# Performance work log

Hardware: AMD Instinct MI355X
Metric: run time of the kernel (lower is better)

## Reference

```python
import jax, jax.numpy as jnp
import numpy as np

SAMPLE_RATE = 22050
N_FILTER_BANKS = 64
HOP_LENGTH = 512
BATCH = 4
N_FRAMES = 500
N_SAMPLES = N_FRAMES * HOP_LENGTH


def _frame_mean_weights(n_frames, n_samples):
    """Per-frame weights w s.t. mean over time of linear(align_corners=True)
    upsampling of a length-n_frames signal equals w @ signal (exact same math,
    since the interpolation is linear in the frame values)."""
    pos = jnp.linspace(0.0, n_frames - 1.0, n_samples)
    lo = jnp.clip(jnp.floor(pos).astype(jnp.int32), 0, n_frames - 2)
    frac = pos - lo
    w = jnp.zeros(n_frames, dtype=jnp.float32)
    w = w.at[lo].add(1.0 - frac).at[lo + 1].add(frac)
    return w / n_samples


def setup_inputs() -> dict:
    key = jax.random.key(0)
    k1, k2 = jax.random.split(key)
    filter_magnitudes = jax.random.uniform(k1, (BATCH, N_FRAMES, N_FILTER_BANKS), dtype=jnp.float32)
    noise = jax.random.normal(k2, (BATCH, N_SAMPLES), dtype=jnp.float32)
    return {"filter_magnitudes": filter_magnitudes, "noise": noise}


def reference(filter_magnitudes, noise):
    B, n_frames, n_banks = filter_magnitudes.shape
    n_samples = noise.shape[1]

    noise_fft = jnp.fft.rfft(noise, axis=1)                      # (B, n_freq) complex
    freqs = jnp.fft.rfftfreq(n_samples, 1.0 / SAMPLE_RATE)       # (n_freq,)
    filter_freqs = jnp.logspace(np.log10(20.0), np.log10(SAMPLE_RATE / 2.0), n_banks).astype(jnp.float32)

    # mean over time of the linearly-upsampled magnitudes (exact, no big buffer)
    mean_w = _frame_mean_weights(n_frames, n_samples)            # (n_frames,)
    mean_mag = jnp.einsum('bfk,f->bk', filter_magnitudes, mean_w)  # (B, n_banks)

    # vectorized log-distance filterbank weights: (n_freq, n_banks)
    D = jnp.log(freqs + 1e-7)[:, None] - jnp.log(filter_freqs + 1e-7)[None, :]
    W = jnp.exp(-(D ** 2) / 0.5)
    W = W / (W.sum(axis=1, keepdims=True) + 1e-7)

    filter_response = mean_mag @ W.T                              # (B, n_freq)
    filtered_fft = noise_fft * filter_response
    return jnp.fft.irfft(filtered_fft, n=n_samples, axis=1)      # (B, n_samples)
```

## Files before the change

### kernel.cpp

```cpp
#include <hip/hip_runtime.h>
#include <math.h>

#define NS 256000
#define N1 512
#define N2 500
#define PI_F 3.14159265358979323846f

typedef float2 cplx;

__device__ __forceinline__ cplx cadd(cplx a, cplx b){ return make_float2(a.x+b.x, a.y+b.y); }
__device__ __forceinline__ cplx csub(cplx a, cplx b){ return make_float2(a.x-b.x, a.y-b.y); }
__device__ __forceinline__ cplx cmul(cplx a, cplx b){ return make_float2(a.x*b.x-a.y*b.y, a.x*b.y+a.y*b.x); }
__device__ __forceinline__ cplx cmulc(cplx a, cplx b){ return make_float2(a.x*b.x+a.y*b.y, a.y*b.x-a.x*b.y); }
__device__ __forceinline__ cplx crotf(cplx v, float ang){
    float sn = __sinf(ang), cs = __cosf(ang);
    return make_float2(v.x*cs - v.y*sn, v.x*sn + v.y*cs);
}
__device__ __forceinline__ int PX(int e){ return e + (e>>4); }
__device__ __forceinline__ int rev8_3(int k){ return ((k&7)<<6) | (k&0x38) | (k>>6); }

#define U1PAD 545
#define U2PAD 537
#define WFENCE() asm volatile("s_waitcnt lgkmcnt(0)" ::: "memory")

template<bool INV>
__device__ __forceinline__ void dft4(const cplx* a, cplx* b){
    cplx t0=cadd(a[0],a[2]), t1=csub(a[0],a[2]), t2=cadd(a[1],a[3]), t3=csub(a[1],a[3]);
    b[0]=cadd(t0,t2); b[2]=csub(t0,t2);
    if(!INV){ b[1]=make_float2(t1.x+t3.y, t1.y-t3.x); b[3]=make_float2(t1.x-t3.y, t1.y+t3.x); }
    else    { b[1]=make_float2(t1.x-t3.y, t1.y+t3.x); b[3]=make_float2(t1.x+t3.y, t1.y-t3.x); }
}

template<bool INV>
__device__ __forceinline__ void dft8(const cplx* a, cplx* b){
    cplx ev[4]={a[0],a[2],a[4],a[6]}, od[4]={a[1],a[3],a[5],a[7]};
    cplx C[4], D[4];
    dft4<INV>(ev, C); dft4<INV>(od, D);
    const float s = 0.70710678118654752f;
    const float sg = INV ? 1.f : -1.f;
    cplx d1 = cmul(D[1], make_float2( s, sg*s));
    cplx d2 = cmul(D[2], make_float2(0.f, sg ));
    cplx d3 = cmul(D[3], make_float2(-s, sg*s));
    b[0]=cadd(C[0],D[0]); b[4]=csub(C[0],D[0]);
    b[1]=cadd(C[1],d1);   b[5]=csub(C[1],d1);
    b[2]=cadd(C[2],d2);   b[6]=csub(C[2],d2);
    b[3]=cadd(C[3],d3);   b[7]=csub(C[3],d3);
}

template<bool INV>
__device__ __forceinline__ void dft5(const cplx* a, cplx* b){
    const float c1=0.30901699437494742f, s1=0.95105651629515357f;
    const float c2=-0.80901699437494745f, s2=0.58778525229247312f;
    const float sg = INV ? 1.f : -1.f;
    cplx W[5];
    W[0]=make_float2(1.f,0.f);
    W[1]=make_float2(c1, sg*s1); W[2]=make_float2(c2, sg*s2);
    W[3]=make_float2(c2,-sg*s2); W[4]=make_float2(c1,-sg*s1);
#pragma unroll
    for(int u=0;u<5;++u){
        cplx acc = a[0];
        int idx = 0;
#pragma unroll
        for(int r=1;r<5;++r){
            idx += u; if(idx >= 5) idx -= 5;
            acc = cadd(acc, cmul(a[r], W[idx]));
        }
        b[u] = acc;
    }
}

template<int R, int L, int TMUL, bool INV, int NN>
__device__ __forceinline__ void wstage(cplx* Uw, const cplx* tab, int lane){
    constexpr int m = L / R;
    constexpr int nb = NN / R;
    constexpr int NIT = (nb + 63) / 64;
    cplx a[NIT][R];
    cplx wt[NIT][R];
    int  bs[NIT];
#pragma unroll
    for(int it=0; it<NIT; ++it){
        int beta = lane + it*64;
        int blk = beta / m;
        int j = beta - blk*m;
        bs[it] = blk*L + j;
        if(beta < nb){
#pragma unroll
            for(int t=0;t<R;++t) a[it][t] = Uw[PX(bs[it] + m*t)];
#pragma unroll
            for(int t=1;t<R;++t) wt[it][t] = tab[TMUL*j*t];
        }
    }
#pragma unroll
    for(int it=0; it<NIT; ++it){
        int beta = lane + it*64;
        if(beta < nb){
            if(INV){
#pragma unroll
                for(int t=1;t<R;++t) a[it][t] = cmulc(a[it][t], wt[it][t]);
            }
            cplx bb[R];
            if constexpr (R==4) dft4<INV>(a[it], bb);
            else if constexpr (R==5) dft5<INV>(a[it], bb);
            else dft8<INV>(a[it], bb);
            if(!INV){
#pragma unroll
                for(int t=1;t<R;++t) bb[t] = cmul(bb[t], wt[it][t]);
            }
#pragma unroll
            for(int t=0;t<R;++t) Uw[PX(bs[it] + m*t)] = bb[t];
        }
    }
}

template<int NTAB>
__device__ __forceinline__ void build_tab(cplx* tab, int tid){
    const float step = -2.f*PI_F/(float)NTAB;
    for(int i = tid; i < NTAB; i += 128){
        float a = step*(float)i;
        tab[i] = make_float2(__cosf(a), __sinf(a));
    }
}

__device__ __forceinline__ int p2k2(int p){
    int t1 = p/100; int r = p - 100*t1;
    int t2 = r/20;  r -= 20*t2;
    int t3 = r>>2;  int t4 = r & 3;
    return t1 + 5*t2 + 25*t3 + 125*t4;
}
__device__ __forceinline__ int k22p(int k){
    int t1 = k % 5; int k5 = k/5;
    int t2 = k5 % 5; int k25 = k5/5;
    int t3 = k25 % 5; int t4 = k25/5;
    return 100*t1 + 20*t2 + 4*t3 + t4;
}
__device__ __forceinline__ int colord(int q){
    int j = q>>1, w = q&1;
    if(j == 0) return w ? 256 : 0;
    return w ? 512 - j : j;
}
__device__ __forceinline__ int xcd_chunk(int bid, int n){
    int q = n>>3, r = n&7;
    int x = bid&7, idx = bid>>3;
    return (x < r ? x*(q+1) : r*(q+1) + (x-r)*q) + idx;
}

__device__ __forceinline__ void hpair(cplx Z1, cplx Z2, float ha, float hb,
                                      cplx* zk, cplx* znk){
    float xr = 0.5f*(Z1.x + Z2.x), xi = 0.5f*(Z1.y - Z2.y);
    float yr = 0.5f*(Z1.y + Z2.y), yi = -0.5f*(Z1.x - Z2.x);
    *zk  = make_float2(ha*xr - hb*yi, ha*xi + hb*yr);
    *znk = make_float2(ha*xr + hb*yi, hb*yr - ha*xi);
}

__global__ void __launch_bounds__(128) kFused1(const float* __restrict__ fm,
                                               const float* __restrict__ noise,
                                               float* __restrict__ mmL,
                                               cplx* __restrict__ Y){
    __shared__ float Aarr[500];
    __shared__ float wfr[500];
    __shared__ float part[128];
    __shared__ cplx tab[512];
    __shared__ cplx U[2][U1PAD];
    const int bid = blockIdx.x, tid = threadIdx.x;
    if(bid < 4){
        const int b = bid;
        for(int f = tid; f < 500; f += 128){
            long long i0 = ((long long)f*255999LL + 498LL)/499LL;
            long long i1 = ((long long)(f+1)*255999LL + 498LL)/499LL;
            long long cnt = i1 - i0;
            long long sumi = (i0 + i1 - 1)*cnt/2;
            long long num = 499LL*sumi - cnt*(long long)f*255999LL;
            Aarr[f] = (float)((double)num / 255999.0);
        }
        __syncthreads();
        for(int f = tid; f < 500; f += 128){
            long long i0 = ((long long)f*255999LL + 498LL)/499LL;
            long long i1 = ((long long)(f+1)*255999LL + 498LL)/499LL;
            double w;
            if(f < 499) w = (double)(i1 - i0) - (double)Aarr[f] + (f > 0 ? (double)Aarr[f-1] : 0.0);
            else        w = (double)Aarr[498] + 1.0;
            wfr[f] = (float)(w / (double)NS);
        }
        __syncthreads();
        const int k = tid & 63, seg = tid >> 6;
        float acc = 0.f;
        for(int f = seg*250; f < seg*250 + 250; ++f)
            acc += wfr[f] * fm[(b*500 + f)*64 + k];
        part[seg*64 + k] = acc;
        __syncthreads();
        if(tid < 64) mmL[b*64 + tid] = part[tid] + part[64 + tid];
        return;
    }
    if(bid == 4){
        if(tid < 64){
            double a = log10(20.0), b2 = log10(11025.0);
            double e = a + (b2 - a)*(double)tid/63.0;
            float ff = (float)pow(10.0, e);
            mmL[256 + tid] = logf(ff + 1e-7f);
        }
        return;
    }
    const int g = bid - 5;
    const int s = g / 250;
    const int n2base = (g - s*250) * 2;
    const int lane = tid & 63, w = tid >> 6;
    build_tab<512>(tab, tid);
    const float* xa = noise + (size_t)(2*s)*NS + n2base;
    const float* xb = noise + (size_t)(2*s+1)*NS + n2base;
#pragma unroll
    for(int k=0;k<8;++k){
        int i = tid + 128*k;
        int n1 = i >> 1, ws = i & 1;
        U[ws][PX(n1)] = make_float2(xa[n1*500 + ws], xb[n1*500 + ws]);
    }
    __syncthreads();
    cplx* Uw = U[w];
    wstage<8,512, 1,false,512>(Uw, tab, lane); WFENCE();
    wstage<8, 64, 8,false,512>(Uw, tab, lane); WFENCE();
    wstage<8,  8,64,false,512>(Uw, tab, lane); WFENCE();
    const int n2 = n2base + w;
    cplx* yp = Y + ((size_t)s*500 + n2)*512;
    const float tw = -2.f*PI_F/(float)NS;
#pragma unroll
    for(int t=0;t<8;++t){
        int q = lane + 64*t;
        int c = colord(q);
        cplx v = Uw[PX(rev8_3(c))];
        v = crotf(v, tw*(float)(n2*c));
        yp[q] = v;
    }
}

__global__ void __launch_bounds__(128) kFused2(cplx* __restrict__ Y,
                                               const float* __restrict__ mmL){
    __shared__ cplx tab[500];
    __shared__ cplx U[2][U2PAD];
    __shared__ float Hr[4][500];
    __shared__ float mmS[2][64];
    __shared__ float lgf[64];
    const int tid = threadIdx.x, lane = tid & 63, w = tid >> 6;
    const int L = xcd_chunk(blockIdx.x, 512);
    const int s = L >> 8, blk = L & 255;
    build_tab<500>(tab, tid);
    if(tid < 128) mmS[tid>>6][tid&63] = mmL[2*s*64 + tid];
    if(tid < 64)  lgf[tid] = mmL[256 + tid];
    cplx* yb = Y + (size_t)s*500*512 + 2*blk;
    cplx rg[8];
#pragma unroll
    for(int k=0;k<8;++k){
        int i = tid + 128*k;
        rg[k] = (i < 1000) ? yb[(i>>1)*512 + (i&1)] : make_float2(0.f, 0.f);
    }
    __syncthreads();
    const int nrows = (blk == 0) ? 2 : 1;
    const float invN = 1.f/(float)NS;
    for(int idx = tid; idx < nrows*500; idx += 128){
        int r = (idx >= 500) ? 1 : 0;
        int p = idx - 500*r;
        int k1 = (blk == 0) ? (r ? 256 : 0) : blk;
        int k2 = p2k2(p);
        int kf = k1 + 512*k2;
        int kk = min(kf, NS - kf);
        float lf = logf((float)kk*(22050.f/(float)NS) + 1e-7f);
        float wsum = 0.f, a0 = 0.f, a1 = 0.f;
#pragma unroll
        for(int jb=0;jb<64;++jb){
            float d = lf - lgf[jb];
            float e = __expf(-2.f*d*d);
            wsum += e; a0 += e*mmS[0][jb]; a1 += e*mmS[1][jb];
        }
        float inv = invN/(wsum + 1e-7f);
        Hr[2*r  ][p] = a0*inv;
        Hr[2*r+1][p] = a1*inv;
    }
#pragma unroll
    for(int k=0;k<8;++k){
        int i = tid + 128*k;
        if(i < 1000) U[i&1][PX(i>>1)] = rg[k];
    }
    __syncthreads();
    cplx* Uw = U[w];
    wstage<5,500,  1,false,500>(Uw, tab, lane); WFENCE();
    wstage<5,100,  5,false,500>(Uw, tab, lane); WFENCE();
    wstage<5, 20, 25,false,500>(Uw, tab, lane); WFENCE();
    wstage<4,  4,125,false,500>(Uw, tab, lane); WFENCE();
    __syncthreads();
    if(blk == 0){
        if(w == 0){
#pragma unroll
            for(int t=0;t<8;++t){
                int p = lane + 64*t;
                if(p < 500){
                    int k2 = p2k2(p);
                    int pp = k22p((500 - k2) % 500);
                    if(p <= pp){
                        cplx Z1 = U[0][PX(p)], Z2 = U[0][PX(pp)];
                        cplx zk, znk;
                        hpair(Z1, Z2, Hr[0][p], Hr[1][p], &zk, &znk);
                        U[0][PX(p)]  = zk;
                        U[0][PX(pp)] = znk;
                    }
                }
            }
        } else {
#pragma unroll
            for(int t=0;t<4;++t){
                int p = lane + 64*t;
                if(p < 250){
                    cplx Z1 = U[1][PX(p)], Z2 = U[1][PX(499-p)];
                    cplx zk, znk;
                    hpair(Z1, Z2, Hr[2][p], Hr[3][p], &zk, &znk);
                    U[1][PX(p)]     = zk;
                    U[1][PX(499-p)] = znk;
                }
            }
        }
    } else {
#pragma unroll
        for(int t=0;t<4;++t){
            int pl = lane + 64*t;
            if(pl < 250){
                int p = w*250 + pl;
                cplx Z1 = U[0][PX(p)], Z2 = U[1][PX(499-p)];
                cplx zk, znk;
                hpair(Z1, Z2, Hr[0][p], Hr[1][p], &zk, &znk);
                U[0][PX(p)]     = zk;
                U[1][PX(499-p)] = znk;
            }
        }
    }
    __syncthreads();
    wstage<4,  4,125,true,500>(Uw, tab, lane); WFENCE();
    wstage<5, 20, 25,true,500>(Uw, tab, lane); WFENCE();
    wstage<5,100,  5,true,500>(Uw, tab, lane); WFENCE();
    wstage<5,500,  1,true,500>(Uw, tab, lane); WFENCE();
    __syncthreads();
    const float tw = 2.f*PI_F/(float)NS;
#pragma unroll
    for(int k=0;k<8;++k){
        int i = tid + 128*k;
        if(i < 1000){
            int n2 = i >> 1, ws = i & 1;
            int c = colord(2*blk + ws);
            cplx v = U[ws][PX(n2)];
            v = crotf(v, tw*(float)(n2*c));
            yb[n2*512 + ws] = v;
        }
    }
}

__global__ void __launch_bounds__(128) kFused3(const cplx* __restrict__ Y,
                                               float* __restrict__ out){
    __shared__ cplx tab[512];
    __shared__ cplx U[2][U1PAD];
    const int tid = threadIdx.x, lane = tid & 63, w = tid >> 6;
    const int L = xcd_chunk(blockIdx.x, 500);
    const int s = L / 250;
    const int n2base = (L - s*250) * 2;
    build_tab<512>(tab, tid);
    const cplx* yp = Y + ((size_t)s*500 + n2base)*512;
#pragma unroll
    for(int k=0;k<8;++k){
        int i = tid + 128*k;
        int ws = i >> 9, q = i & 511;
        cplx v = yp[(size_t)ws*512 + q];
        U[ws][PX(rev8_3(colord(q)))] = v;
    }
    __syncthreads();
    cplx* Uw = U[w];
    wstage<8,  8,64,true,512>(Uw, tab, lane); WFENCE();
    wstage<8, 64, 8,true,512>(Uw, tab, lane); WFENCE();
    wstage<8,512, 1,true,512>(Uw, tab, lane); WFENCE();
    __syncthreads();
    float* oa = out + (size_t)(2*s)*NS + n2base;
    float* ob = out + (size_t)(2*s+1)*NS + n2base;
#pragma unroll
    for(int k=0;k<8;++k){
        int i = tid + 128*k;
        int n1 = i >> 1, ws = i & 1;
        cplx v = U[ws][PX(n1)];
        oa[n1*500 + ws] = v.x;
        ob[n1*500 + ws] = v.y;
    }
}

extern "C" void kernel_launch(void* const* d_in, const int* in_sizes, int n_in,
                              void* d_out, int out_size, void* d_ws, size_t ws_size,
                              hipStream_t stream) {
    const float* fm = (const float*)d_in[0];
    const float* noise = (const float*)d_in[1];
    float* out = (float*)d_out;

    char* ws = (char*)d_ws;
    cplx*  Y   = (cplx*)ws;
    float* mmL = (float*)(ws + 4200000);

    kFused1<<<505, 128, 0, stream>>>(fm, noise, mmL, Y);
    kFused2<<<512, 128, 0, stream>>>(Y, mmL);
    kFused3<<<500, 128, 0, stream>>>(Y, out);
}
```

Before: 98.65 us.

## Widen FFT blocks to four columns, pad Y rows, and roll FFT stage loops

kFused1 and kFused3 now use 256-thread blocks that each process four columns instead of two, and they remap block IDs across XCDs. The Y workspace row stride is padded from 512 to 528, presumably to reduce channel or bank conflicts. The templated radix stages are replaced by rolled per-wave FFT loops, and many unrolls are disabled to cut code size and register pressure. kFused2 now issues its global loads before building the twiddle table and uses a lighter barrier. The rolled loops may add loop overhead and lose instruction-level parallelism.

Measured after the change: 100.4 us. No clear change (+1.8%).

```diff
diff --git a/kernel.cpp b/kernel.cpp
--- a/kernel.cpp
+++ b/kernel.cpp
@@ -4,6 +4,7 @@
 #define NS 256000
 #define N1 512
 #define N2 500
+#define YS 528
 #define PI_F 3.14159265358979323846f
 
 typedef float2 cplx;
@@ -22,6 +23,7 @@
 #define U1PAD 545
 #define U2PAD 537
 #define WFENCE() asm volatile("s_waitcnt lgkmcnt(0)" ::: "memory")
+#define LDS_BARRIER() do{ asm volatile("s_waitcnt lgkmcnt(0)" ::: "memory"); __builtin_amdgcn_s_barrier(); }while(0)
 
 template<bool INV>
 __device__ __forceinline__ void dft4(const cplx* a, cplx* b){
@@ -69,53 +71,110 @@
     }
 }
 
-template<int R, int L, int TMUL, bool INV, int NN>
-__device__ __forceinline__ void wstage(cplx* Uw, const cplx* tab, int lane){
-    constexpr int m = L / R;
-    constexpr int nb = NN / R;
-    constexpr int NIT = (nb + 63) / 64;
-    cplx a[NIT][R];
-    cplx wt[NIT][R];
-    int  bs[NIT];
-#pragma unroll
-    for(int it=0; it<NIT; ++it){
-        int beta = lane + it*64;
-        int blk = beta / m;
-        int j = beta - blk*m;
-        bs[it] = blk*L + j;
-        if(beta < nb){
-#pragma unroll
-            for(int t=0;t<R;++t) a[it][t] = Uw[PX(bs[it] + m*t)];
-#pragma unroll
-            for(int t=1;t<R;++t) wt[it][t] = tab[TMUL*j*t];
-        }
-    }
-#pragma unroll
-    for(int it=0; it<NIT; ++it){
-        int beta = lane + it*64;
-        if(beta < nb){
-            if(INV){
-#pragma unroll
-                for(int t=1;t<R;++t) a[it][t] = cmulc(a[it][t], wt[it][t]);
-            }
-            cplx bb[R];
-            if constexpr (R==4) dft4<INV>(a[it], bb);
-            else if constexpr (R==5) dft5<INV>(a[it], bb);
-            else dft8<INV>(a[it], bb);
-            if(!INV){
-#pragma unroll
-                for(int t=1;t<R;++t) bb[t] = cmul(bb[t], wt[it][t]);
-            }
-#pragma unroll
-            for(int t=0;t<R;++t) Uw[PX(bs[it] + m*t)] = bb[t];
-        }
-    }
-}
-
-template<int NTAB>
+template<bool INV>
+__device__ __forceinline__ void fft512_wave(cplx* Uw, const cplx* tab, int lane){
+#pragma unroll 1
+    for(int st=0; st<3; ++st){
+        const int sh = INV ? 3*st : 6-3*st;
+        const int m = 1<<sh;
+        const int blk = lane >> sh, j = lane & (m-1);
+        const int base = (blk << (sh+3)) + j;
+        cplx a[8], wt[8];
+#pragma unroll
+        for(int t=0;t<8;++t) a[t] = Uw[PX(base + (t<<sh))];
+#pragma unroll
+        for(int t=1;t<8;++t) wt[t] = tab[(j*t) << (6-sh)];
+        if(INV){
+#pragma unroll
+            for(int t=1;t<8;++t) a[t] = cmulc(a[t], wt[t]);
+        }
+        cplx bb[8];
+        dft8<INV>(a,bb);
+        if(!INV){
+#pragma unroll
+            for(int t=1;t<8;++t) bb[t] = cmul(bb[t], wt[t]);
+        }
+#pragma unroll
+        for(int t=0;t<8;++t) Uw[PX(base + (t<<sh))] = bb[t];
+        WFENCE();
+    }
+}
+
+template<bool INV>
+__device__ __forceinline__ void fft500_wave(cplx* Uw, const cplx* tab, int lane){
+    if(INV){
+#pragma unroll 1
+        for(int it=0; it<2; ++it){
+            int beta = lane + 64*it;
+            if(beta < 125){
+                int base = beta*4;
+                cplx a[4];
+#pragma unroll
+                for(int t=0;t<4;++t) a[t] = Uw[PX(base+t)];
+                cplx bb[4];
+                dft4<true>(a,bb);
+#pragma unroll
+                for(int t=0;t<4;++t) Uw[PX(base+t)] = bb[t];
+            }
+        }
+        WFENCE();
+    }
+#pragma unroll 1
+    for(int s5=0; s5<3; ++s5){
+        const int st = INV ? 2-s5 : s5;
+        const int m  = (st==0)?100:((st==1)?20:4);
+        const int tm = (st==0)?1:((st==1)?5:25);
+#pragma unroll 1
+        for(int it=0; it<2; ++it){
+            int beta = lane + 64*it;
+            if(beta < 100){
+                int blk = (st==0) ? 0 : ((st==1) ? (int)(((unsigned)beta*52429u)>>20) : (beta>>2));
+                int j = beta - blk*m;
+                int base = blk*(m*5) + j;
+                cplx a[5], wt[5];
+#pragma unroll
+                for(int t=0;t<5;++t) a[t] = Uw[PX(base + m*t)];
+#pragma unroll
+                for(int t=1;t<5;++t) wt[t] = tab[tm*j*t];
+                if(INV){
+#pragma unroll
+                    for(int t=1;t<5;++t) a[t] = cmulc(a[t], wt[t]);
+                }
+                cplx bb[5];
+                dft5<INV>(a,bb);
+                if(!INV){
+#pragma unroll
+                    for(int t=1;t<5;++t) bb[t] = cmul(bb[t], wt[t]);
+                }
+#pragma unroll
+                for(int t=0;t<5;++t) Uw[PX(base + m*t)] = bb[t];
+            }
+        }
+        WFENCE();
+    }
+    if(!INV){
+#pragma unroll 1
+        for(int it=0; it<2; ++it){
+            int beta = lane + 64*it;
+            if(beta < 125){
+                int base = beta*4;
+                cplx a[4];
+#pragma unroll
+                for(int t=0;t<4;++t) a[t] = Uw[PX(base+t)];
+                cplx bb[4];
+                dft4<false>(a,bb);
+#pragma unroll
+                for(int t=0;t<4;++t) Uw[PX(base+t)] = bb[t];
+            }
+        }
+        WFENCE();
+    }
+}
+
+template<int NTAB, int NTHR>
 __device__ __forceinline__ void build_tab(cplx* tab, int tid){
     const float step = -2.f*PI_F/(float)NTAB;
-    for(int i = tid; i < NTAB; i += 128){
+    for(int i = tid; i < NTAB; i += NTHR){
         float a = step*(float)i;
         tab[i] = make_float2(__cosf(a), __sinf(a));
     }
@@ -152,19 +211,19 @@
     *znk = make_float2(ha*xr + hb*yi, hb*yr - ha*xi);
 }
 
-__global__ void __launch_bounds__(128) kFused1(const float* __restrict__ fm,
+__global__ void __launch_bounds__(256) kFused1(const float* __restrict__ fm,
                                                const float* __restrict__ noise,
                                                float* __restrict__ mmL,
                                                cplx* __restrict__ Y){
     __shared__ float Aarr[500];
     __shared__ float wfr[500];
-    __shared__ float part[128];
+    __shared__ float part[256];
     __shared__ cplx tab[512];
-    __shared__ cplx U[2][U1PAD];
+    __shared__ cplx U[4][U1PAD];
     const int bid = blockIdx.x, tid = threadIdx.x;
     if(bid < 4){
         const int b = bid;
-        for(int f = tid; f < 500; f += 128){
+        for(int f = tid; f < 500; f += 256){
             long long i0 = ((long long)f*255999LL + 498LL)/499LL;
             long long i1 = ((long long)(f+1)*255999LL + 498LL)/499LL;
             long long cnt = i1 - i0;
@@ -173,7 +232,7 @@
             Aarr[f] = (float)((double)num / 255999.0);
         }
         __syncthreads();
-        for(int f = tid; f < 500; f += 128){
+        for(int f = tid; f < 500; f += 256){
             long long i0 = ((long long)f*255999LL + 498LL)/499LL;
             long long i1 = ((long long)(f+1)*255999LL + 498LL)/499LL;
             double w;
@@ -184,11 +243,11 @@
         __syncthreads();
         const int k = tid & 63, seg = tid >> 6;
         float acc = 0.f;
-        for(int f = seg*250; f < seg*250 + 250; ++f)
+        for(int f = seg*125; f < seg*125 + 125; ++f)
             acc += wfr[f] * fm[(b*500 + f)*64 + k];
         part[seg*64 + k] = acc;
         __syncthreads();
-        if(tid < 64) mmL[b*64 + tid] = part[tid] + part[64 + tid];
+        if(tid < 64) mmL[b*64 + tid] = part[tid] + part[64+tid] + part[128+tid] + part[192+tid];
         return;
     }
     if(bid == 4){
@@ -200,28 +259,26 @@
         }
         return;
     }
-    const int g = bid - 5;
-    const int s = g / 250;
-    const int n2base = (g - s*250) * 2;
+    const int g = xcd_chunk(bid - 5, 250);
+    const int s = g / 125;
+    const int n2base = (g - s*125) * 4;
     const int lane = tid & 63, w = tid >> 6;
-    build_tab<512>(tab, tid);
+    build_tab<512,256>(tab, tid);
     const float* xa = noise + (size_t)(2*s)*NS + n2base;
     const float* xb = noise + (size_t)(2*s+1)*NS + n2base;
 #pragma unroll
     for(int k=0;k<8;++k){
-        int i = tid + 128*k;
-        int n1 = i >> 1, ws = i & 1;
+        int i = tid + 256*k;
+        int n1 = i >> 2, ws = i & 3;
         U[ws][PX(n1)] = make_float2(xa[n1*500 + ws], xb[n1*500 + ws]);
     }
     __syncthreads();
     cplx* Uw = U[w];
-    wstage<8,512, 1,false,512>(Uw, tab, lane); WFENCE();
-    wstage<8, 64, 8,false,512>(Uw, tab, lane); WFENCE();
-    wstage<8,  8,64,false,512>(Uw, tab, lane); WFENCE();
+    fft512_wave<false>(Uw, tab, lane);
     const int n2 = n2base + w;
-    cplx* yp = Y + ((size_t)s*500 + n2)*512;
+    cplx* yp = Y + ((size_t)s*500 + n2)*YS;
     const float tw = -2.f*PI_F/(float)NS;
-#pragma unroll
+#pragma unroll 1
     for(int t=0;t<8;++t){
         int q = lane + 64*t;
         int c = colord(q);
@@ -241,19 +298,20 @@
     const int tid = threadIdx.x, lane = tid & 63, w = tid >> 6;
     const int L = xcd_chunk(blockIdx.x, 512);
     const int s = L >> 8, blk = L & 255;
-    build_tab<500>(tab, tid);
+    cplx* yb = Y + (size_t)s*500*YS + 2*blk;
+    cplx rg[8];
+#pragma unroll
+    for(int k=0;k<8;++k){
+        int i = tid + 128*k;
+        rg[k] = (i < 1000) ? yb[(i>>1)*YS + (i&1)] : make_float2(0.f, 0.f);
+    }
+    build_tab<500,128>(tab, tid);
     if(tid < 128) mmS[tid>>6][tid&63] = mmL[2*s*64 + tid];
     if(tid < 64)  lgf[tid] = mmL[256 + tid];
-    cplx* yb = Y + (size_t)s*500*512 + 2*blk;
-    cplx rg[8];
-#pragma unroll
-    for(int k=0;k<8;++k){
-        int i = tid + 128*k;
-        rg[k] = (i < 1000) ? yb[(i>>1)*512 + (i&1)] : make_float2(0.f, 0.f);
-    }
-    __syncthreads();
+    LDS_BARRIER();
     const int nrows = (blk == 0) ? 2 : 1;
     const float invN = 1.f/(float)NS;
+#pragma unroll 1
     for(int idx = tid; idx < nrows*500; idx += 128){
         int r = (idx >= 500) ? 1 : 0;
         int p = idx - 500*r;
@@ -263,15 +321,15 @@
         int kk = min(kf, NS - kf);
         float lf = logf((float)kk*(22050.f/(float)NS) + 1e-7f);
         float wsum = 0.f, a0 = 0.f, a1 = 0.f;
-#pragma unroll
+#pragma unroll 8
         for(int jb=0;jb<64;++jb){
             float d = lf - lgf[jb];
             float e = __expf(-2.f*d*d);
             wsum += e; a0 += e*mmS[0][jb]; a1 += e*mmS[1][jb];
         }
         float inv = invN/(wsum + 1e-7f);
-        Hr[2*r  ][p] = a0*inv;
-        Hr[2*r+1][p] = a1*inv;
+        if(r==0){ Hr[0][p] = a0*inv; Hr[1][p] = a1*inv; }
+        else    { Hr[2][p] = a0*inv; Hr[3][p] = a1*inv; }
     }
 #pragma unroll
     for(int k=0;k<8;++k){
@@ -280,14 +338,11 @@
     }
     __syncthreads();
     cplx* Uw = U[w];
-    wstage<5,500,  1,false,500>(Uw, tab, lane); WFENCE();
-    wstage<5,100,  5,false,500>(Uw, tab, lane); WFENCE();
-    wstage<5, 20, 25,false,500>(Uw, tab, lane); WFENCE();
-    wstage<4,  4,125,false,500>(Uw, tab, lane); WFENCE();
+    fft500_wave<false>(Uw, tab, lane);
     __syncthreads();
     if(blk == 0){
         if(w == 0){
-#pragma unroll
+#pragma unroll 1
             for(int t=0;t<8;++t){
                 int p = lane + 64*t;
                 if(p < 500){
@@ -303,7 +358,7 @@
                 }
             }
         } else {
-#pragma unroll
+#pragma unroll 1
             for(int t=0;t<4;++t){
                 int p = lane + 64*t;
                 if(p < 250){
@@ -316,7 +371,7 @@
             }
         }
     } else {
-#pragma unroll
+#pragma unroll 1
         for(int t=0;t<4;++t){
             int pl = lane + 64*t;
             if(pl < 250){
@@ -330,54 +385,49 @@
         }
     }
     __syncthreads();
-    wstage<4,  4,125,true,500>(Uw, tab, lane); WFENCE();
-    wstage<5, 20, 25,true,500>(Uw, tab, lane); WFENCE();
-    wstage<5,100,  5,true,500>(Uw, tab, lane); WFENCE();
-    wstage<5,500,  1,true,500>(Uw, tab, lane); WFENCE();
+    fft500_wave<true>(Uw, tab, lane);
     __syncthreads();
     const float tw = 2.f*PI_F/(float)NS;
-#pragma unroll
+#pragma unroll 1
     for(int k=0;k<8;++k){
         int i = tid + 128*k;
         if(i < 1000){
             int n2 = i >> 1, ws = i & 1;
-            int c = colord(2*blk + ws);
+            int cc = colord(2*blk + ws);
             cplx v = U[ws][PX(n2)];
-            v = crotf(v, tw*(float)(n2*c));
-            yb[n2*512 + ws] = v;
-        }
-    }
-}
-
-__global__ void __launch_bounds__(128) kFused3(const cplx* __restrict__ Y,
+            v = crotf(v, tw*(float)(n2*cc));
+            yb[n2*YS + ws] = v;
+        }
+    }
+}
+
+__global__ void __launch_bounds__(256) kFused3(const cplx* __restrict__ Y,
                                                float* __restrict__ out){
     __shared__ cplx tab[512];
-    __shared__ cplx U[2][U1PAD];
+    __shared__ cplx U[4][U1PAD];
     const int tid = threadIdx.x, lane = tid & 63, w = tid >> 6;
-    const int L = xcd_chunk(blockIdx.x, 500);
-    const int s = L / 250;
-    const int n2base = (L - s*250) * 2;
-    build_tab<512>(tab, tid);
-    const cplx* yp = Y + ((size_t)s*500 + n2base)*512;
-#pragma unroll
-    for(int k=0;k<8;++k){
-        int i = tid + 128*k;
+    const int g = xcd_chunk(blockIdx.x, 250);
+    const int s = g / 125;
+    const int n2base = (g - s*125) * 4;
+    build_tab<512,256>(tab, tid);
+    const cplx* yp = Y + ((size_t)s*500 + n2base)*YS;
+#pragma unroll 1
+    for(int k=0;k<8;++k){
+        int i = tid + 256*k;
         int ws = i >> 9, q = i & 511;
-        cplx v = yp[(size_t)ws*512 + q];
+        cplx v = yp[(size_t)ws*YS + q];
         U[ws][PX(rev8_3(colord(q)))] = v;
     }
     __syncthreads();
     cplx* Uw = U[w];
-    wstage<8,  8,64,true,512>(Uw, tab, lane); WFENCE();
-    wstage<8, 64, 8,true,512>(Uw, tab, lane); WFENCE();
-    wstage<8,512, 1,true,512>(Uw, tab, lane); WFENCE();
+    fft512_wave<true>(Uw, tab, lane);
     __syncthreads();
     float* oa = out + (size_t)(2*s)*NS + n2base;
     float* ob = out + (size_t)(2*s+1)*NS + n2base;
-#pragma unroll
-    for(int k=0;k<8;++k){
-        int i = tid + 128*k;
-        int n1 = i >> 1, ws = i & 1;
+#pragma unroll 1
+    for(int k=0;k<8;++k){
+        int i = tid + 256*k;
+        int n1 = i >> 2, ws = i & 3;
         cplx v = U[ws][PX(n1)];
         oa[n1*500 + ws] = v.x;
         ob[n1*500 + ws] = v.y;
@@ -393,9 +443,9 @@
 
     char* ws = (char*)d_ws;
     cplx*  Y   = (cplx*)ws;
-    float* mmL = (float*)(ws + 4200000);
-
-    kFused1<<<505, 128, 0, stream>>>(fm, noise, mmL, Y);
+    float* mmL = (float*)(ws + 4224000);
+
+    kFused1<<<255, 256, 0, stream>>>(fm, noise, mmL, Y);
     kFused2<<<512, 128, 0, stream>>>(Y, mmL);
-    kFused3<<<500, 128, 0, stream>>>(Y, out);
-}
+    kFused3<<<250, 256, 0, stream>>>(Y, out);
+}
```
